# Optimization experiments

Measured on AMD Instinct MI355X. Metric: run time of the kernel, lower is better.

The kernel has to match this reference:

```python
import jax, jax.numpy as jnp
import numpy as np

N_NODES, N_GRAPHS, N_EDGES = 40960, 1024, 163840


def setup_inputs() -> dict:
    key = jax.random.key(0)
    ks = jax.random.split(key, 40)
    w = lambda k, s: jax.random.normal(k, s, jnp.float32) * 0.05
    inp = {
        "x": jax.random.normal(ks[0], (N_NODES, 78), jnp.float32),
        "edge_index": jax.random.randint(ks[1], (2, N_EDGES), 0, N_NODES, jnp.int32),
        "batch": jnp.repeat(jnp.arange(N_GRAPHS, dtype=jnp.int32), N_NODES // N_GRAPHS),
        "target1": jax.random.normal(ks[2], (N_GRAPHS, 750, 20), jnp.float32),
        "target2": jax.random.randint(ks[3], (N_GRAPHS, 750), 0, 26, jnp.int32),
        # GCN layers
        "W1": w(ks[4], (78, 78)), "b1": jnp.zeros((78,), jnp.float32),
        "W2": w(ks[5], (78, 156)), "b2": jnp.zeros((156,), jnp.float32),
        "W3": w(ks[6], (156, 312)), "b3": jnp.zeros((312,), jnp.float32),
        "Wg1": w(ks[7], (312, 1024)), "bg1": jnp.zeros((1024,), jnp.float32),
        "Wg2": w(ks[8], (1024, 128)), "bg2": jnp.zeros((128,), jnp.float32),
        # protein branch
        "emb": w(ks[9], (26, 128)),
        "Wc2": w(ks[10], (32, 750, 8)), "bc2": jnp.zeros((32,), jnp.float32),
        "Wxt2": w(ks[11], (32 * 121, 128)), "bxt2": jnp.zeros((128,), jnp.float32),
        "Wc1": w(ks[12], (32, 750, 8)), "bc1": jnp.zeros((32,), jnp.float32),
        "Wxt1": w(ks[13], (416, 128)), "bxt1": jnp.zeros((128,), jnp.float32),
        # fusion head
        "Wf1": w(ks[14], (384, 1024)), "bf1": jnp.zeros((1024,), jnp.float32),
        "Wf2": w(ks[15], (1024, 512)), "bf2": jnp.zeros((512,), jnp.float32),
        "Wo": w(ks[16], (512, 1)), "bo": jnp.zeros((1,), jnp.float32),
    }
    return inp


def _conv1d(x, w, b):
    # x: [B, C_in, L], w: [C_out, C_in, K] -> [B, C_out, L-K+1]
    y = jax.lax.conv_general_dilated(x, w, (1,), "VALID",
                                     dimension_numbers=("NCH", "OIH", "NCH"))
    return y + b[None, :, None]


def reference(x, edge_index, batch, target1, target2,
              W1, b1, W2, b2, W3, b3, Wg1, bg1, Wg2, bg2,
              emb, Wc2, bc2, Wxt2, bxt2, Wc1, bc1, Wxt1, bxt1,
              Wf1, bf1, Wf2, bf2, Wo, bo):
    N = x.shape[0]
    loop = jnp.arange(N, dtype=edge_index.dtype)
    src = jnp.concatenate([edge_index[0], loop])  # message source j
    dst = jnp.concatenate([edge_index[1], loop])  # aggregation target i
    # symmetric GCN normalization with self-loops (degree from dst, as in PyG)
    deg = jnp.zeros((N,), x.dtype).at[dst].add(1.0)
    dinv = jax.lax.rsqrt(deg)  # deg >= 1 due to self loops
    norm = (dinv[src] * dinv[dst])[:, None]

    def gcn(h, W, b):
        m = (h @ W)[src] * norm
        return jax.ops.segment_sum(m, dst, num_segments=N) + b

    h = jax.nn.relu(gcn(x, W1, b1))
    h = jax.nn.relu(gcn(h, W2, b2))
    h = jax.nn.relu(gcn(h, W3, b3))
    # global max pool per graph
    g = jax.ops.segment_max(h, batch, num_segments=N_GRAPHS)
    g = jax.nn.relu(g @ Wg1 + bg1)
    g = g @ Wg2 + bg2  # dropout is identity at inference

    # protein branch 2: embedding -> conv1d over channels=750
    e = emb[target2]                         # [B, 750, 128]
    xt2 = _conv1d(e, Wc2, bc2)               # [B, 32, 121]
    xt2 = xt2.reshape(-1, 32 * 121) @ Wxt2 + bxt2

    # protein branch 1: raw float features
    xt1 = _conv1d(target1, Wc1, bc1)         # [B, 32, 13]
    xt1 = xt1.reshape(-1, 416) @ Wxt1 + bxt1

    xc = jnp.concatenate([g, xt1, xt2], axis=1)  # [B, 384]
    xc = jax.nn.relu(xc @ Wf1 + bf1)
    xc = jax.nn.relu(xc @ Wf2 + bf2)
    return xc @ Wo + bo
```

## Files before the change

kernel.cpp:

```cpp
#include <hip/hip_runtime.h>
#include <hip/hip_bf16.h>

#define NN 40960
#define NE 163840
#define NB 1024

typedef __attribute__((ext_vector_type(8))) short short8;
typedef __attribute__((ext_vector_type(4))) float floatx4;

__device__ inline unsigned short f2bf(float f) {
    union { float f; unsigned u; } v; v.f = f;
    unsigned r = v.u + 0x7fffu + ((v.u >> 16) & 1u);
    return (unsigned short)(r >> 16);
}
__device__ inline float bf2f(unsigned short s) {
    union { unsigned u; float f; } v; v.u = ((unsigned)s) << 16; return v.f;
}

static const size_t o_dinv = 0, o_g312 = 40960, o_g1024 = 360448, o_xc = 1409024,
                    o_f1 = 1802240, o_f2 = 2850816, o_b1v = 3375104, o_b2v = 3375232,
                    o_iws = 3375360, o_bufA = 3621124, o_bufB = 16400644;


__global__ void k_hist(const int* __restrict__ dst, int* __restrict__ cnt) {
    int e = blockIdx.x * 256 + threadIdx.x;
    if (e < NE) atomicAdd(&cnt[dst[e]], 1);
}

__global__ __launch_bounds__(1024) void k_scan1(const int* __restrict__ cnt, int* __restrict__ offTmp,
                                                int* __restrict__ blockSum, float* __restrict__ dinv) {
    __shared__ int lds[1024];
    int tid = threadIdx.x;
    int i = blockIdx.x * 1024 + tid;
    int v = cnt[i];
    dinv[i] = rsqrtf((float)v + 1.0f);
    lds[tid] = v;
    __syncthreads();
    for (int s = 1; s < 1024; s <<= 1) {
        int t = (tid >= s) ? lds[tid - s] : 0;
        __syncthreads();
        lds[tid] += t;
        __syncthreads();
    }
    offTmp[i] = lds[tid] - v;
    if (tid == 1023) blockSum[blockIdx.x] = lds[1023];
}

__global__ __launch_bounds__(64) void k_scan2(const int* __restrict__ blockSum, int* __restrict__ blockOff) {
    int l = threadIdx.x;
    int s = (l < 40) ? blockSum[l] : 0;
    int orig = s;
    for (int d = 1; d < 64; d <<= 1) {
        int t = __shfl_up(s, d);
        if (l >= d) s += t;
    }
    if (l < 40) blockOff[l] = s - orig;
}

__global__ __launch_bounds__(1024) void k_scan3(int* __restrict__ off, int* __restrict__ cur,
                                                const int* __restrict__ blockOff) {
    int i = blockIdx.x * 1024 + threadIdx.x;
    int o = off[i] + blockOff[blockIdx.x];
    off[i] = o;
    cur[i] = o;
    if (i == NN - 1) off[NN] = NE;
}

__global__ void k_fill(const int* __restrict__ ei, int* __restrict__ cur, int* __restrict__ srcOut) {
    int e = blockIdx.x * 256 + threadIdx.x;
    if (e >= NE) return;
    int s = ei[e], d = ei[NE + e];
    int pos = atomicAdd(&cur[d], 1);
    srcOut[pos] = s;
}

__global__ __launch_bounds__(256) void k_cvt_wt(const float* __restrict__ W1, const float* __restrict__ W2,
                                                const float* __restrict__ W3, const float* __restrict__ Wg1,
                                                const float* __restrict__ Wg2, const float* __restrict__ Wf1,
                                                const float* __restrict__ Wf2, unsigned short* __restrict__ dst) {
    const int cum[8]  = {0, 128, 320, 640, 1664, 1792, 2816, 3328};
    const int KP[7]   = {96, 96, 160, 320, 1024, 384, 1024};
    const int KB[7]   = {78, 78, 156, 312, 1024, 384, 1024};
    const int NNm[7]  = {78, 156, 312, 1024, 128, 1024, 512};
    const size_t OFF[7] = {0, 12288, 30720, 81920, 409600, 540672, 933888};
    int m = 0;
    int bx = blockIdx.x;
    while (m < 6 && bx >= cum[m + 1]) m++;
    int r = bx - cum[m];
    const float* src = (m == 0) ? W1 : (m == 1) ? W2 : (m == 2) ? W3 : (m == 3) ? Wg1
                     : (m == 4) ? Wg2 : (m == 5) ? Wf1 : Wf2;
    int kp = KP[m], kb = KB[m], nn = NNm[m];
    unsigned short* d = dst + OFF[m] + (size_t)r * kp;
    for (int k = threadIdx.x; k < kp; k += 256) {
        float v = (r < nn && k < kb) ? src[(size_t)k * nn + r] : 0.f;
        d[k] = f2bf(v);
    }
}

__global__ __launch_bounds__(256) void k_cvt_flat(const float* __restrict__ in, unsigned short* __restrict__ out, long n) {
    long i = ((long)blockIdx.x * 256 + threadIdx.x) * 8;
    if (i + 8 > n) return;
    float4 a = *(const float4*)(in + i);
    float4 b = *(const float4*)(in + i + 4);
    short8 sv;
    sv[0] = (short)f2bf(a.x); sv[1] = (short)f2bf(a.y); sv[2] = (short)f2bf(a.z); sv[3] = (short)f2bf(a.w);
    sv[4] = (short)f2bf(b.x); sv[5] = (short)f2bf(b.y); sv[6] = (short)f2bf(b.z); sv[7] = (short)f2bf(b.w);
    *(short8*)(out + i) = sv;
}

__global__ void k_agg_x(const float* __restrict__ x, const float* __restrict__ dinv,
                        const int* __restrict__ off, const int* __restrict__ srcs,
                        unsigned short* __restrict__ out) {
    int n = blockIdx.x;
    int f = threadIdx.x;
    if (f >= 96) return;
    if (f >= 78) { out[(size_t)n * 96 + f] = 0; return; }
    float di = dinv[n];
    float acc = x[(size_t)n * 78 + f] * di * di;
    int e0 = off[n], e1 = off[n + 1];
    int e = e0;
    for (; e + 4 <= e1; e += 4) {
        int s0 = srcs[e], s1 = srcs[e + 1], s2 = srcs[e + 2], s3 = srcs[e + 3];
        float d0 = dinv[s0], d1 = dinv[s1], d2 = dinv[s2], d3 = dinv[s3];
        float v0 = x[(size_t)s0 * 78 + f];
        float v1 = x[(size_t)s1 * 78 + f];
        float v2 = x[(size_t)s2 * 78 + f];
        float v3 = x[(size_t)s3 * 78 + f];
        acc += v0 * (d0 * di) + v1 * (d1 * di) + v2 * (d2 * di) + v3 * (d3 * di);
    }
    for (; e < e1; e++) {
        int s = srcs[e];
        acc += x[(size_t)s * 78 + f] * (dinv[s] * di);
    }
    out[(size_t)n * 96 + f] = f2bf(acc);
}

__global__ void k_agg16(const unsigned short* __restrict__ h, const float* __restrict__ dinv,
                        const int* __restrict__ off, const int* __restrict__ srcs,
                        unsigned short* __restrict__ out, int F) {
    int n = blockIdx.x;
    int f = threadIdx.x;
    if (f >= F) return;
    float di = dinv[n];
    float acc = bf2f(h[(size_t)n * F + f]) * di * di;
    int e0 = off[n], e1 = off[n + 1];
    int e = e0;
    for (; e + 4 <= e1; e += 4) {
        int s0 = srcs[e], s1 = srcs[e + 1], s2 = srcs[e + 2], s3 = srcs[e + 3];
        float d0 = dinv[s0], d1 = dinv[s1], d2 = dinv[s2], d3 = dinv[s3];
        float v0 = bf2f(h[(size_t)s0 * F + f]);
        float v1 = bf2f(h[(size_t)s1 * F + f]);
        float v2 = bf2f(h[(size_t)s2 * F + f]);
        float v3 = bf2f(h[(size_t)s3 * F + f]);
        acc += v0 * (d0 * di) + v1 * (d1 * di) + v2 * (d2 * di) + v3 * (d3 * di);
    }
    for (; e < e1; e++) {
        int s = srcs[e];
        acc += bf2f(h[(size_t)s * F + f]) * (dinv[s] * di);
    }
    out[(size_t)n * F + f] = f2bf(acc);
}

__global__ void k_segmax16(const unsigned short* __restrict__ h, unsigned short* __restrict__ g) {
    int gr = blockIdx.x, f = threadIdx.x;
    if (f >= 320) return;
    if (f >= 312) { g[(size_t)gr * 320 + f] = 0; return; }
    float m = 0.0f;
    const unsigned short* base = h + (size_t)gr * 40 * 312 + f;
    for (int i = 0; i < 40; i++) m = fmaxf(m, bf2f(base[(size_t)i * 312]));
    g[(size_t)gr * 320 + f] = f2bf(m);
}

#define LDST 72
template <bool ABF16, bool OUTBF16, bool ATOMIC, bool RELU_OUT>
__global__ __launch_bounds__(256) void gemm_bt(const void* __restrict__ Av, const unsigned short* __restrict__ Bt,
                                               const float* __restrict__ bias, void* __restrict__ Cv,
                                               int Nn, int Npad, int Kpad,
                                               int lda, int ldb, int ldc, int ksplit) {
    __shared__ __align__(16) unsigned short As[64 * LDST];
    __shared__ __align__(16) unsigned short Bs[64 * LDST];
    const float* Af = (const float*)Av;
    const unsigned short* A16 = (const unsigned short*)Av;
    float* Cf = (float*)Cv;
    unsigned short* C16 = (unsigned short*)Cv;
    int bn0 = blockIdx.x * 64;
    int bm0 = blockIdx.y * 64;
    int k0 = blockIdx.z * ksplit;
    int kend = k0 + ksplit; if (kend > Kpad) kend = Kpad;
    int tid = threadIdx.x;
    int w = tid >> 6, l = tid & 63, q = l >> 4, r = l & 15;
    int wr = w >> 1, wc = w & 1;

    floatx4 acc[2][2];
#pragma unroll
    for (int i = 0; i < 2; i++)
#pragma unroll
        for (int c = 0; c < 2; c++) acc[i][c] = (floatx4)0.0f;

    int mA = tid >> 2, kcA = (tid & 3) * 8;
    int nB = tid >> 2, kcB = (tid & 3) * 8;
    int gmA = bm0 + mA;
    int gnB = bn0 + nB;

    for (int kt = k0; kt < kend; kt += 32) {
        if (ABF16) {
            *(short8*)&As[mA * LDST + kcA] = *(const short8*)(A16 + (size_t)gmA * lda + kt + kcA);
        } else {
            const float* Ap = Af + (size_t)gmA * lda + kt + kcA;
            float av[8];
#pragma unroll
            for (int j = 0; j < 4; j++) {
                float2 p = *(const float2*)(Ap + j * 2);
                av[j * 2] = p.x; av[j * 2 + 1] = p.y;
            }
            short8 sv;
#pragma unroll
            for (int j = 0; j < 8; j++) sv[j] = (short)f2bf(av[j]);
            *(short8*)&As[mA * LDST + kcA] = sv;
        }
        *(short8*)&Bs[nB * LDST + kcB] = *(const short8*)(Bt + (size_t)gnB * ldb + kt + kcB);
        __syncthreads();
        short8 a0 = *(const short8*)&As[(wr * 32 + r) * LDST + q * 8];
        short8 a1 = *(const short8*)&As[(wr * 32 + 16 + r) * LDST + q * 8];
        short8 b0 = *(const short8*)&Bs[(wc * 32 + r) * LDST + q * 8];
        short8 b1 = *(const short8*)&Bs[(wc * 32 + 16 + r) * LDST + q * 8];
        acc[0][0] = __builtin_amdgcn_mfma_f32_16x16x32_bf16(a0, b0, acc[0][0], 0, 0, 0);
        acc[0][1] = __builtin_amdgcn_mfma_f32_16x16x32_bf16(a0, b1, acc[0][1], 0, 0, 0);
        acc[1][0] = __builtin_amdgcn_mfma_f32_16x16x32_bf16(a1, b0, acc[1][0], 0, 0, 0);
        acc[1][1] = __builtin_amdgcn_mfma_f32_16x16x32_bf16(a1, b1, acc[1][1], 0, 0, 0);
        __syncthreads();
    }

#pragma unroll
    for (int c2 = 0; c2 < 2; c2++) {
        int col = bn0 + wc * 32 + c2 * 16 + r;
        if (col >= Npad) continue;
        bool live = col < Nn;
        float bv = (bias && live) ? bias[col] : 0.f;
#pragma unroll
        for (int i = 0; i < 2; i++) {
#pragma unroll
            for (int v = 0; v < 4; v++) {
                int row = bm0 + wr * 32 + i * 16 + q * 4 + v;
                float val = live ? (acc[i][c2][v] + bv) : 0.f;
                if (RELU_OUT) val = fmaxf(val, 0.f);
                if (OUTBF16) {
                    C16[(size_t)row * ldc + col] = live ? f2bf(val) : (unsigned short)0;
                } else if (live) {
                    if (ATOMIC) atomicAdd(&Cf[(size_t)row * ldc + col], val);
                    else Cf[(size_t)row * ldc + col] = val;
                }
            }
        }
    }
}

template <int OM>
__global__ __launch_bounds__(256) void gemm_mfma_batch(const float* __restrict__ A, const float* __restrict__ B,
                                                       void* __restrict__ Cv,
                                                       int M, int Nn, int K, int ldc,
                                                       long sB, long sC) {
    __shared__ __align__(16) unsigned short As[64 * LDST];
    __shared__ __align__(16) unsigned short Bs[64 * LDST];
    const float* Bm = B + (size_t)blockIdx.z * sB;
    unsigned short* C16 = (unsigned short*)Cv + (size_t)blockIdx.z * sC;
    int bn0 = blockIdx.x * 64;
    int bm0 = blockIdx.y * 64;
    int tid = threadIdx.x;
    int w = tid >> 6, l = tid & 63, q = l >> 4, r = l & 15;
    int wr = w >> 1, wc = w & 1;

    floatx4 acc[2][2];
#pragma unroll
    for (int i = 0; i < 2; i++)
#pragma unroll
        for (int c = 0; c < 2; c++) acc[i][c] = (floatx4)0.0f;

    int mA = tid >> 2, kcA = (tid & 3) * 8;
    int nB = tid >> 2, kcB = (tid & 3) * 8;
    int gmA = bm0 + mA;
    int gnB = bn0 + nB;

    for (int kt = 0; kt < K; kt += 32) {
        {
            float av[8];
            const float* Ap = A + (size_t)gmA * K + kt + kcA;
            if (gmA < M) {
#pragma unroll
                for (int j = 0; j < 4; j++) {
                    float2 p = *(const float2*)(Ap + j * 2);
                    av[j * 2] = p.x; av[j * 2 + 1] = p.y;
                }
            } else {
#pragma unroll
                for (int j = 0; j < 8; j++) av[j] = 0.f;
            }
            short8 sv;
#pragma unroll
            for (int j = 0; j < 8; j++) sv[j] = (short)f2bf(av[j]);
            *(short8*)&As[mA * LDST + kcA] = sv;
        }
        {
            short8 sv;
#pragma unroll
            for (int j = 0; j < 8; j++) {
                int gk = kt + kcB + j;
                float v = (gnB < Nn) ? Bm[(size_t)gk * Nn + gnB] : 0.f;
                sv[j] = (short)f2bf(v);
            }
            *(short8*)&Bs[nB * LDST + kcB] = sv;
        }
        __syncthreads();
        short8 a0 = *(const short8*)&As[(wr * 32 + r) * LDST + q * 8];
        short8 a1 = *(const short8*)&As[(wr * 32 + 16 + r) * LDST + q * 8];
        short8 b0 = *(const short8*)&Bs[(wc * 32 + r) * LDST + q * 8];
        short8 b1 = *(const short8*)&Bs[(wc * 32 + 16 + r) * LDST + q * 8];
        acc[0][0] = __builtin_amdgcn_mfma_f32_16x16x32_bf16(a0, b0, acc[0][0], 0, 0, 0);
        acc[0][1] = __builtin_amdgcn_mfma_f32_16x16x32_bf16(a0, b1, acc[0][1], 0, 0, 0);
        acc[1][0] = __builtin_amdgcn_mfma_f32_16x16x32_bf16(a1, b0, acc[1][0], 0, 0, 0);
        acc[1][1] = __builtin_amdgcn_mfma_f32_16x16x32_bf16(a1, b1, acc[1][1], 0, 0, 0);
        __syncthreads();
    }

#pragma unroll
    for (int c = 0; c < 2; c++) {
        int col = bn0 + wc * 32 + c * 16 + r;
        if (col >= Nn) continue;
#pragma unroll
        for (int i = 0; i < 2; i++) {
#pragma unroll
            for (int v = 0; v < 4; v++) {
                int row = bm0 + wr * 32 + i * 16 + q * 4 + v;
                if (row >= M) continue;
                if (OM == 1) C16[(size_t)row * ldc + col] = f2bf(acc[i][c][v]);
                else C16[(size_t)col * ldc + row * 20 + blockIdx.z] = f2bf(acc[i][c][v]);
            }
        }
    }
}

__global__ void k_rowinit(float* __restrict__ C, int ldc, const float* __restrict__ bias) {
    C[(size_t)blockIdx.x * ldc + threadIdx.x] = bias[threadIdx.x];
}

__global__ __launch_bounds__(256) void k_wcr(const float* __restrict__ W, float* __restrict__ Wr) {
    int c = blockIdx.x, j = threadIdx.x;
    Wr[(size_t)c * 256 + j] = W[(size_t)(j >> 3) * 6000 + c * 8 + (j & 7)];
}

__global__ __launch_bounds__(128) void k_T_build(const float* __restrict__ emb, const float* __restrict__ Wxt2,
                                                 float* __restrict__ T) {
    __shared__ float el[128];
    int v = blockIdx.x >> 5, o = blockIdx.x & 31, j = threadIdx.x;
    el[j] = emb[(size_t)v * 128 + j];
    __syncthreads();
    float acc[8] = {};
    for (int l = 0; l < 121; l++) {
        float w = Wxt2[(size_t)(o * 121 + l) * 128 + j];
#pragma unroll
        for (int k = 0; k < 8; k++) acc[k] += el[l + k] * w;
    }
#pragma unroll
    for (int k = 0; k < 8; k++) T[(size_t)(v * 256 + o * 8 + k) * 128 + j] = acc[k];
}

__global__ __launch_bounds__(128) void k_bt_build(const float* __restrict__ Wxt1, float* __restrict__ Bt) {
    int ok = blockIdx.x, t = blockIdx.y, j = threadIdx.x;
    int o = ok >> 3, k = ok & 7, lpos = t - k;
    float v = (lpos >= 0 && lpos < 13) ? Wxt1[(size_t)(o * 13 + lpos) * 128 + j] : 0.f;
    Bt[(size_t)(t * 256 + ok) * 128 + j] = v;
}

__global__ __launch_bounds__(128) void k_u_gather16(const int* __restrict__ t2, const unsigned short* __restrict__ U,
                                                    const float* __restrict__ b2v, float* __restrict__ xc) {
    __shared__ int offs[752];
    __shared__ float red[8][128];
    int b = blockIdx.x, tid = threadIdx.x;
    int rg = tid >> 4, lane = tid & 15;
    const int* t2b = t2 + (size_t)b * 750;
    for (int i = tid; i < 750; i += 128) offs[i] = i * 3328 + t2b[i] * 128;
    __syncthreads();
    float a[8] = {};
#pragma unroll 4
    for (int i = rg; i < 750; i += 8) {
        short8 v = *(const short8*)&U[(size_t)offs[i] + lane * 8];
#pragma unroll
        for (int c = 0; c < 8; c++) a[c] += bf2f((unsigned short)v[c]);
    }
#pragma unroll
    for (int c = 0; c < 8; c++) red[rg][lane * 8 + c] = a[c];
    __syncthreads();
    float s = b2v[tid];
#pragma unroll
    for (int g = 0; g < 8; g++) s += red[g][tid];
    xc[(size_t)b * 384 + 256 + tid] = s;
}

__global__ void k_bias_init(const float* __restrict__ bxt1, const float* __restrict__ bxt2,
                            float* __restrict__ b1v, float* __restrict__ b2v) {
    int j = threadIdx.x;
    b1v[j] = bxt1[j];
    b2v[j] = bxt2[j];
}

template <int L>
__global__ __launch_bounds__(128) void k_bias_acc(const float* __restrict__ bc, const float* __restrict__ W,
                                                  float* __restrict__ out) {
    int o = blockIdx.x, j = threadIdx.x;
    const float* p = W + (size_t)o * L * 128 + j;
    float t = 0.f;
    for (int l = 0; l < L; l++) t += p[(size_t)l * 128];
    atomicAdd(&out[j], bc[o] * t);
}

__global__ __launch_bounds__(64) void k_final(const float* __restrict__ f2, const float* __restrict__ Wo,
                                              const float* __restrict__ bo, float* __restrict__ out) {
    int b = blockIdx.x, lane = threadIdx.x;
    float s = 0.f;
    for (int j = lane; j < 512; j += 64) s += fmaxf(f2[(size_t)b * 512 + j], 0.f) * Wo[j];
    for (int off = 32; off; off >>= 1) s += __shfl_down(s, off);
    if (lane == 0) out[b] = s + bo[0];
}

extern "C" void kernel_launch(void* const* d_in, const int* in_sizes, int n_in,
                              void* d_out, int out_size, void* d_ws, size_t ws_size,
                              hipStream_t stream) {
    const float* x    = (const float*)d_in[0];
    const int*   ei   = (const int*)d_in[1];
    const float* t1   = (const float*)d_in[3];
    const int*   t2   = (const int*)d_in[4];
    const float* W1   = (const float*)d_in[5];
    const float* b1   = (const float*)d_in[6];
    const float* W2   = (const float*)d_in[7];
    const float* b2   = (const float*)d_in[8];
    const float* W3   = (const float*)d_in[9];
    const float* b3   = (const float*)d_in[10];
    const float* Wg1  = (const float*)d_in[11];
    const float* bg1  = (const float*)d_in[12];
    const float* Wg2  = (const float*)d_in[13];
    const float* bg2  = (const float*)d_in[14];
    const float* emb  = (const float*)d_in[15];
    const float* Wc2  = (const float*)d_in[16];
    const float* bc2  = (const float*)d_in[17];
    const float* Wxt2 = (const float*)d_in[18];
    const float* bxt2 = (const float*)d_in[19];
    const float* Wc1  = (const float*)d_in[20];
    const float* bc1  = (const float*)d_in[21];
    const float* Wxt1 = (const float*)d_in[22];
    const float* bxt1 = (const float*)d_in[23];
    const float* Wf1  = (const float*)d_in[24];
    const float* bf1  = (const float*)d_in[25];
    const float* Wf2  = (const float*)d_in[26];
    const float* bf2  = (const float*)d_in[27];
    const float* Wo   = (const float*)d_in[28];
    const float* bo   = (const float*)d_in[29];
    float* out = (float*)d_out;

    float* ws = (float*)d_ws;
    float* dinv  = ws + o_dinv;
    unsigned short* g312b = (unsigned short*)(ws + o_g312);
    unsigned short* g1024b = (unsigned short*)(ws + o_g1024);
    float* xc    = ws + o_xc;
    unsigned short* f1b = (unsigned short*)(ws + o_f1);
    float* f2    = ws + o_f2;
    float* b1v   = ws + o_b1v;
    float* b2v   = ws + o_b2v;
    int* csrOff  = (int*)(ws + o_iws);
    int* csrCur  = csrOff + (NN + 1);
    int* csrSrc  = csrCur + NN;
    int* blockSum = (int*)(ws + o_f1 + 600000);
    int* blockOff = blockSum + 40;
    float* bufA  = ws + o_bufA;
    float* bufB  = ws + o_bufB;
    float* T    = bufA;
    unsigned short* U16  = (unsigned short*)(bufA + 851968);
    unsigned short* Vt16 = (unsigned short*)(bufA + 2200000);
    unsigned short* Wt   = (unsigned short*)(bufA + 3200000);
    float* Wc2r = bufA + 4000000;
    float* Wc1r = bufA + 4200000;
    float* Btb  = bufA + 4400000;
    unsigned short* aggb = (unsigned short*)bufB;
    unsigned short* h16  = (unsigned short*)(bufB + 5500000);
    unsigned short* t1b  = (unsigned short*)bufB;

    unsigned short* W1t  = Wt + 0;
    unsigned short* W2t  = Wt + 12288;
    unsigned short* W3t  = Wt + 30720;
    unsigned short* Wg1t = Wt + 81920;
    unsigned short* Wg2t = Wt + 409600;
    unsigned short* Wf1t = Wt + 540672;
    unsigned short* Wf2t = Wt + 933888;

    hipMemsetAsync(csrCur, 0, NN * sizeof(int), stream);
    k_hist<<<NE / 256, 256, 0, stream>>>(ei + NE, csrCur);
    k_scan1<<<40, 1024, 0, stream>>>(csrCur, csrOff, blockSum, dinv);
    k_scan2<<<1, 64, 0, stream>>>(blockSum, blockOff);
    k_scan3<<<40, 1024, 0, stream>>>(csrOff, csrCur, blockOff);
    k_fill<<<NE / 256, 256, 0, stream>>>(ei, csrCur, csrSrc);
    k_cvt_wt<<<3328, 256, 0, stream>>>(W1, W2, W3, Wg1, Wg2, Wf1, Wf2, Wt);

    k_agg_x<<<NN, 128, 0, stream>>>(x, dinv, csrOff, csrSrc, aggb);
    gemm_bt<true, true, false, true><<<dim3(2, 640, 1), 256, 0, stream>>>(
        aggb, W1t, b1, h16, 78, 96, 96, 96, 96, 96, 96);
    k_agg16<<<NN, 128, 0, stream>>>(h16, dinv, csrOff, csrSrc, aggb, 96);
    gemm_bt<true, true, false, true><<<dim3(3, 640, 1), 256, 0, stream>>>(
        aggb, W2t, b2, h16, 156, 160, 96, 96, 96, 160, 96);
    k_agg16<<<NN, 192, 0, stream>>>(h16, dinv, csrOff, csrSrc, aggb, 160);
    gemm_bt<true, true, false, true><<<dim3(5, 640, 1), 256, 0, stream>>>(
        aggb, W3t, b3, h16, 312, 312, 160, 160, 160, 312, 160);
    k_segmax16<<<NB, 320, 0, stream>>>(h16, g312b);
    k_cvt_flat<<<7500, 256, 0, stream>>>(t1, t1b, 15360000L);
    gemm_bt<true, true, false, true><<<dim3(16, 16, 1), 256, 0, stream>>>(
        g312b, Wg1t, bg1, g1024b, 1024, 1024, 320, 320, 320, 1024, 320);

    k_bias_init<<<1, 128, 0, stream>>>(bxt1, bxt2, b1v, b2v);
    k_bias_acc<13><<<32, 128, 0, stream>>>(bc1, Wxt1, b1v);
    k_bias_acc<121><<<32, 128, 0, stream>>>(bc2, Wxt2, b2v);

    k_rowinit<<<NB, 128, 0, stream>>>(xc + 0, 384, bg2);
    gemm_bt<true, false, true, false><<<dim3(2, 16, 8), 256, 0, stream>>>(
        g1024b, Wg2t, nullptr, xc + 0, 128, 128, 1024, 1024, 1024, 384, 128);

    k_wcr<<<750, 256, 0, stream>>>(Wc2, Wc2r);
    k_T_build<<<26 * 32, 128, 0, stream>>>(emb, Wxt2, T);
    gemm_mfma_batch<1><<<dim3(2, 12, 26), 256, 0, stream>>>(Wc2r, T, U16, 750, 128, 256, 3328, 32768, 128);
    k_u_gather16<<<NB, 128, 0, stream>>>(t2, U16, b2v, xc);

    k_wcr<<<750, 256, 0, stream>>>(Wc1, Wc1r);
    k_bt_build<<<dim3(256, 20), 128, 0, stream>>>(Wxt1, Btb);
    hipMemsetAsync(Vt16, 0, (size_t)128 * 15008 * 2, stream);
    gemm_mfma_batch<2><<<dim3(2, 12, 20), 256, 0, stream>>>(Wc1r, Btb, Vt16, 750, 128, 256, 15008, 32768, 0);
    k_rowinit<<<NB, 128, 0, stream>>>(xc + 128, 384, b1v);
    gemm_bt<true, false, true, false><<<dim3(2, 16, 32), 256, 0, stream>>>(
        t1b, Vt16, nullptr, xc + 128, 128, 128, 15008, 15000, 15008, 384, 480);

    gemm_bt<false, true, false, true><<<dim3(16, 16, 1), 256, 0, stream>>>(
        xc, Wf1t, bf1, f1b, 1024, 1024, 384, 384, 384, 1024, 384);
    k_rowinit<<<NB, 512, 0, stream>>>(f2, 512, bf2);
    gemm_bt<true, false, true, false><<<dim3(8, 16, 4), 256, 0, stream>>>(
        f1b, Wf2t, nullptr, f2, 512, 512, 1024, 1024, 1024, 512, 256);
    k_final<<<NB, 64, 0, stream>>>(f2, Wo, bo, out);
}
```

Measured before the change: 499.7 us.

## Vectorize GCN aggregation, fuse small init kernels, drop target1 bf16 pre-conversion

The GCN aggregation kernels now process two features per thread with packed bf16 pairs and float2 loads, which halves the thread count per node. Several tiny launches are merged: both conv-weight reorders, both bias accumulations, and the three row-init kernels. The separate fp32-to-bf16 conversion pass over target1 is removed, and the split-K GEMM instead reads fp32 directly with a new K-limit bound for the ragged tail. The aim is to cut launch overhead and one full read/write pass over the large target1 tensor, at the cost of converting inside the GEMM and reading fp32 there, which is twice the bytes of bf16.

Result: faster. 463.3 us (-7.3%).

```diff
diff --git a/kernel.cpp b/kernel.cpp
--- a/kernel.cpp
+++ b/kernel.cpp
@@ -16,11 +16,13 @@
 __device__ inline float bf2f(unsigned short s) {
     union { unsigned u; float f; } v; v.u = ((unsigned)s) << 16; return v.f;
 }
+__device__ inline unsigned pack2bf(float lo, float hi) {
+    return (unsigned)f2bf(lo) | ((unsigned)f2bf(hi) << 16);
+}
 
 static const size_t o_dinv = 0, o_g312 = 40960, o_g1024 = 360448, o_xc = 1409024,
                     o_f1 = 1802240, o_f2 = 2850816, o_b1v = 3375104, o_b2v = 3375232,
                     o_iws = 3375360, o_bufA = 3621124, o_bufB = 16400644;
-
 
 __global__ void k_hist(const int* __restrict__ dst, int* __restrict__ cnt) {
     int e = blockIdx.x * 256 + threadIdx.x;
@@ -97,68 +99,69 @@
     }
 }
 
-__global__ __launch_bounds__(256) void k_cvt_flat(const float* __restrict__ in, unsigned short* __restrict__ out, long n) {
-    long i = ((long)blockIdx.x * 256 + threadIdx.x) * 8;
-    if (i + 8 > n) return;
-    float4 a = *(const float4*)(in + i);
-    float4 b = *(const float4*)(in + i + 4);
-    short8 sv;
-    sv[0] = (short)f2bf(a.x); sv[1] = (short)f2bf(a.y); sv[2] = (short)f2bf(a.z); sv[3] = (short)f2bf(a.w);
-    sv[4] = (short)f2bf(b.x); sv[5] = (short)f2bf(b.y); sv[6] = (short)f2bf(b.z); sv[7] = (short)f2bf(b.w);
-    *(short8*)(out + i) = sv;
-}
-
-__global__ void k_agg_x(const float* __restrict__ x, const float* __restrict__ dinv,
-                        const int* __restrict__ off, const int* __restrict__ srcs,
-                        unsigned short* __restrict__ out) {
+__global__ __launch_bounds__(64) void k_agg_x(const float* __restrict__ x, const float* __restrict__ dinv,
+                                              const int* __restrict__ off, const int* __restrict__ srcs,
+                                              unsigned* __restrict__ out) {
     int n = blockIdx.x;
     int f = threadIdx.x;
-    if (f >= 96) return;
-    if (f >= 78) { out[(size_t)n * 96 + f] = 0; return; }
+    if (f >= 48) return;
+    if (f >= 39) { out[(size_t)n * 48 + f] = 0; return; }
     float di = dinv[n];
-    float acc = x[(size_t)n * 78 + f] * di * di;
+    float2 sv = *(const float2*)&x[(size_t)n * 78 + 2 * f];
+    float a0 = sv.x * di * di, a1 = sv.y * di * di;
     int e0 = off[n], e1 = off[n + 1];
     int e = e0;
     for (; e + 4 <= e1; e += 4) {
         int s0 = srcs[e], s1 = srcs[e + 1], s2 = srcs[e + 2], s3 = srcs[e + 3];
-        float d0 = dinv[s0], d1 = dinv[s1], d2 = dinv[s2], d3 = dinv[s3];
-        float v0 = x[(size_t)s0 * 78 + f];
-        float v1 = x[(size_t)s1 * 78 + f];
-        float v2 = x[(size_t)s2 * 78 + f];
-        float v3 = x[(size_t)s3 * 78 + f];
-        acc += v0 * (d0 * di) + v1 * (d1 * di) + v2 * (d2 * di) + v3 * (d3 * di);
+        float d0 = dinv[s0] * di, d1 = dinv[s1] * di, d2 = dinv[s2] * di, d3 = dinv[s3] * di;
+        float2 v0 = *(const float2*)&x[(size_t)s0 * 78 + 2 * f];
+        float2 v1 = *(const float2*)&x[(size_t)s1 * 78 + 2 * f];
+        float2 v2 = *(const float2*)&x[(size_t)s2 * 78 + 2 * f];
+        float2 v3 = *(const float2*)&x[(size_t)s3 * 78 + 2 * f];
+        a0 += v0.x * d0 + v1.x * d1 + v2.x * d2 + v3.x * d3;
+        a1 += v0.y * d0 + v1.y * d1 + v2.y * d2 + v3.y * d3;
     }
     for (; e < e1; e++) {
         int s = srcs[e];
-        acc += x[(size_t)s * 78 + f] * (dinv[s] * di);
-    }
-    out[(size_t)n * 96 + f] = f2bf(acc);
-}
-
-__global__ void k_agg16(const unsigned short* __restrict__ h, const float* __restrict__ dinv,
+        float dd = dinv[s] * di;
+        float2 v = *(const float2*)&x[(size_t)s * 78 + 2 * f];
+        a0 += v.x * dd; a1 += v.y * dd;
+    }
+    out[(size_t)n * 48 + f] = pack2bf(a0, a1);
+}
+
+__global__ void k_agg16(const unsigned* __restrict__ h, const float* __restrict__ dinv,
                         const int* __restrict__ off, const int* __restrict__ srcs,
-                        unsigned short* __restrict__ out, int F) {
+                        unsigned* __restrict__ out, int F2) {
     int n = blockIdx.x;
     int f = threadIdx.x;
-    if (f >= F) return;
+    if (f >= F2) return;
     float di = dinv[n];
-    float acc = bf2f(h[(size_t)n * F + f]) * di * di;
+    unsigned s0v = h[(size_t)n * F2 + f];
+    float a0 = bf2f((unsigned short)(s0v & 0xffff)) * di * di;
+    float a1 = bf2f((unsigned short)(s0v >> 16)) * di * di;
     int e0 = off[n], e1 = off[n + 1];
     int e = e0;
     for (; e + 4 <= e1; e += 4) {
         int s0 = srcs[e], s1 = srcs[e + 1], s2 = srcs[e + 2], s3 = srcs[e + 3];
-        float d0 = dinv[s0], d1 = dinv[s1], d2 = dinv[s2], d3 = dinv[s3];
-        float v0 = bf2f(h[(size_t)s0 * F + f]);
-        float v1 = bf2f(h[(size_t)s1 * F + f]);
-        float v2 = bf2f(h[(size_t)s2 * F + f]);
-        float v3 = bf2f(h[(size_t)s3 * F + f]);
-        acc += v0 * (d0 * di) + v1 * (d1 * di) + v2 * (d2 * di) + v3 * (d3 * di);
+        float d0 = dinv[s0] * di, d1 = dinv[s1] * di, d2 = dinv[s2] * di, d3 = dinv[s3] * di;
+        unsigned v0 = h[(size_t)s0 * F2 + f];
+        unsigned v1 = h[(size_t)s1 * F2 + f];
+        unsigned v2 = h[(size_t)s2 * F2 + f];
+        unsigned v3 = h[(size_t)s3 * F2 + f];
+        a0 += bf2f((unsigned short)(v0 & 0xffff)) * d0 + bf2f((unsigned short)(v1 & 0xffff)) * d1
+            + bf2f((unsigned short)(v2 & 0xffff)) * d2 + bf2f((unsigned short)(v3 & 0xffff)) * d3;
+        a1 += bf2f((unsigned short)(v0 >> 16)) * d0 + bf2f((unsigned short)(v1 >> 16)) * d1
+            + bf2f((unsigned short)(v2 >> 16)) * d2 + bf2f((unsigned short)(v3 >> 16)) * d3;
     }
     for (; e < e1; e++) {
         int s = srcs[e];
-        acc += bf2f(h[(size_t)s * F + f]) * (dinv[s] * di);
-    }
-    out[(size_t)n * F + f] = f2bf(acc);
+        float dd = dinv[s] * di;
+        unsigned v = h[(size_t)s * F2 + f];
+        a0 += bf2f((unsigned short)(v & 0xffff)) * dd;
+        a1 += bf2f((unsigned short)(v >> 16)) * dd;
+    }
+    out[(size_t)n * F2 + f] = pack2bf(a0, a1);
 }
 
 __global__ void k_segmax16(const unsigned short* __restrict__ h, unsigned short* __restrict__ g) {
@@ -175,7 +178,7 @@
 template <bool ABF16, bool OUTBF16, bool ATOMIC, bool RELU_OUT>
 __global__ __launch_bounds__(256) void gemm_bt(const void* __restrict__ Av, const unsigned short* __restrict__ Bt,
                                                const float* __restrict__ bias, void* __restrict__ Cv,
-                                               int Nn, int Npad, int Kpad,
+                                               int Nn, int Npad, int Kpad, int Klim,
                                                int lda, int ldb, int ldc, int ksplit) {
     __shared__ __align__(16) unsigned short As[64 * LDST];
     __shared__ __align__(16) unsigned short Bs[64 * LDST];
@@ -208,10 +211,15 @@
         } else {
             const float* Ap = Af + (size_t)gmA * lda + kt + kcA;
             float av[8];
-#pragma unroll
-            for (int j = 0; j < 4; j++) {
-                float2 p = *(const float2*)(Ap + j * 2);
-                av[j * 2] = p.x; av[j * 2 + 1] = p.y;
+            if (kt + kcA + 8 <= Klim) {
+#pragma unroll
+                for (int j = 0; j < 4; j++) {
+                    float2 p = *(const float2*)(Ap + j * 2);
+                    av[j * 2] = p.x; av[j * 2 + 1] = p.y;
+                }
+            } else {
+#pragma unroll
+                for (int j = 0; j < 8; j++) av[j] = (kt + kcA + j < Klim) ? Ap[j] : 0.f;
             }
             short8 sv;
 #pragma unroll
@@ -339,12 +347,12 @@
     }
 }
 
-__global__ void k_rowinit(float* __restrict__ C, int ldc, const float* __restrict__ bias) {
-    C[(size_t)blockIdx.x * ldc + threadIdx.x] = bias[threadIdx.x];
-}
-
-__global__ __launch_bounds__(256) void k_wcr(const float* __restrict__ W, float* __restrict__ Wr) {
-    int c = blockIdx.x, j = threadIdx.x;
+__global__ __launch_bounds__(256) void k_wcr_both(const float* __restrict__ Wc2, const float* __restrict__ Wc1,
+                                                  float* __restrict__ Wc2r, float* __restrict__ Wc1r) {
+    int cc = blockIdx.x, j = threadIdx.x;
+    const float* W = (cc < 750) ? Wc2 : Wc1;
+    float* Wr = (cc < 750) ? Wc2r : Wc1r;
+    int c = (cc < 750) ? cc : cc - 750;
     Wr[(size_t)c * 256 + j] = W[(size_t)(j >> 3) * 6000 + c * 8 + (j & 7)];
 }
 
@@ -403,14 +411,32 @@
     b2v[j] = bxt2[j];
 }
 
-template <int L>
-__global__ __launch_bounds__(128) void k_bias_acc(const float* __restrict__ bc, const float* __restrict__ W,
-                                                  float* __restrict__ out) {
-    int o = blockIdx.x, j = threadIdx.x;
-    const float* p = W + (size_t)o * L * 128 + j;
-    float t = 0.f;
-    for (int l = 0; l < L; l++) t += p[(size_t)l * 128];
-    atomicAdd(&out[j], bc[o] * t);
+__global__ __launch_bounds__(128) void k_bias_acc_both(const float* __restrict__ bc1, const float* __restrict__ Wxt1,
+                                                       float* __restrict__ b1v,
+                                                       const float* __restrict__ bc2, const float* __restrict__ Wxt2,
+                                                       float* __restrict__ b2v) {
+    int b = blockIdx.x, j = threadIdx.x;
+    if (b < 32) {
+        const float* p = Wxt1 + (size_t)b * 13 * 128 + j;
+        float t = 0.f;
+        for (int l = 0; l < 13; l++) t += p[(size_t)l * 128];
+        atomicAdd(&b1v[j], bc1[b] * t);
+    } else {
+        int o = b - 32;
+        const float* p = Wxt2 + (size_t)o * 121 * 128 + j;
+        float t = 0.f;
+        for (int l = 0; l < 121; l++) t += p[(size_t)l * 128];
+        atomicAdd(&b2v[j], bc2[o] * t);
+    }
+}
+
+__global__ __launch_bounds__(768) void k_initC(float* __restrict__ xc, float* __restrict__ f2,
+                                               const float* __restrict__ bg2, const float* __restrict__ b1v,
+                                               const float* __restrict__ bf2) {
+    int b = blockIdx.x, t = threadIdx.x;
+    if (t < 128) xc[(size_t)b * 384 + t] = bg2[t];
+    else if (t < 256) xc[(size_t)b * 384 + t] = b1v[t - 128];
+    else f2[(size_t)b * 512 + t - 256] = bf2[t - 256];
 }
 
 __global__ __launch_bounds__(64) void k_final(const float* __restrict__ f2, const float* __restrict__ Wo,
@@ -479,9 +505,8 @@
     float* Wc2r = bufA + 4000000;
     float* Wc1r = bufA + 4200000;
     float* Btb  = bufA + 4400000;
-    unsigned short* aggb = (unsigned short*)bufB;
-    unsigned short* h16  = (unsigned short*)(bufB + 5500000);
-    unsigned short* t1b  = (unsigned short*)bufB;
+    unsigned* aggb = (unsigned*)bufB;
+    unsigned short* h16 = (unsigned short*)(bufB + 5500000);
 
     unsigned short* W1t  = Wt + 0;
     unsigned short* W2t  = Wt + 12288;
@@ -499,45 +524,40 @@
     k_fill<<<NE / 256, 256, 0, stream>>>(ei, csrCur, csrSrc);
     k_cvt_wt<<<3328, 256, 0, stream>>>(W1, W2, W3, Wg1, Wg2, Wf1, Wf2, Wt);
 
-    k_agg_x<<<NN, 128, 0, stream>>>(x, dinv, csrOff, csrSrc, aggb);
+    k_agg_x<<<NN, 64, 0, stream>>>(x, dinv, csrOff, csrSrc, aggb);
     gemm_bt<true, true, false, true><<<dim3(2, 640, 1), 256, 0, stream>>>(
-        aggb, W1t, b1, h16, 78, 96, 96, 96, 96, 96, 96);
-    k_agg16<<<NN, 128, 0, stream>>>(h16, dinv, csrOff, csrSrc, aggb, 96);
+        aggb, W1t, b1, h16, 78, 96, 96, 96, 96, 96, 96, 96);
+    k_agg16<<<NN, 64, 0, stream>>>((unsigned*)h16, dinv, csrOff, csrSrc, aggb, 48);
     gemm_bt<true, true, false, true><<<dim3(3, 640, 1), 256, 0, stream>>>(
-        aggb, W2t, b2, h16, 156, 160, 96, 96, 96, 160, 96);
-    k_agg16<<<NN, 192, 0, stream>>>(h16, dinv, csrOff, csrSrc, aggb, 160);
+        aggb, W2t, b2, h16, 156, 160, 96, 96, 96, 96, 160, 96);
+    k_agg16<<<NN, 128, 0, stream>>>((unsigned*)h16, dinv, csrOff, csrSrc, aggb, 80);
     gemm_bt<true, true, false, true><<<dim3(5, 640, 1), 256, 0, stream>>>(
-        aggb, W3t, b3, h16, 312, 312, 160, 160, 160, 312, 160);
+        aggb, W3t, b3, h16, 312, 312, 160, 160, 160, 160, 312, 160);
     k_segmax16<<<NB, 320, 0, stream>>>(h16, g312b);
-    k_cvt_flat<<<7500, 256, 0, stream>>>(t1, t1b, 15360000L);
     gemm_bt<true, true, false, true><<<dim3(16, 16, 1), 256, 0, stream>>>(
-        g312b, Wg1t, bg1, g1024b, 1024, 1024, 320, 320, 320, 1024, 320);
+        g312b, Wg1t, bg1, g1024b, 1024, 1024, 320, 320, 320, 320, 1024, 320);
 
     k_bias_init<<<1, 128, 0, stream>>>(bxt1, bxt2, b1v, b2v);
-    k_bias_acc<13><<<32, 128, 0, stream>>>(bc1, Wxt1, b1v);
-    k_bias_acc<121><<<32, 128, 0, stream>>>(bc2, Wxt2, b2v);
-
-    k_rowinit<<<NB, 128, 0, stream>>>(xc + 0, 384, bg2);
+    k_bias_acc_both<<<64, 128, 0, stream>>>(bc1, Wxt1, b1v, bc2, Wxt2, b2v);
+    k_initC<<<NB, 768, 0, stream>>>(xc, f2, bg2, b1v, bf2);
+
     gemm_bt<true, false, true, false><<<dim3(2, 16, 8), 256, 0, stream>>>(
-        g1024b, Wg2t, nullptr, xc + 0, 128, 128, 1024, 1024, 1024, 384, 128);
-
-    k_wcr<<<750, 256, 0, stream>>>(Wc2, Wc2r);
+        g1024b, Wg2t, nullptr, xc + 0, 128, 128, 1024, 1024, 1024, 1024, 384, 128);
+
+    k_wcr_both<<<1500, 256, 0, stream>>>(Wc2, Wc1, Wc2r, Wc1r);
     k_T_build<<<26 * 32, 128, 0, stream>>>(emb, Wxt2, T);
     gemm_mfma_batch<1><<<dim3(2, 12, 26), 256, 0, stream>>>(Wc2r, T, U16, 750, 128, 256, 3328, 32768, 128);
     k_u_gather16<<<NB, 128, 0, stream>>>(t2, U16, b2v, xc);
 
-    k_wcr<<<750, 256, 0, stream>>>(Wc1, Wc1r);
     k_bt_build<<<dim3(256, 20), 128, 0, stream>>>(Wxt1, Btb);
     hipMemsetAsync(Vt16, 0, (size_t)128 * 15008 * 2, stream);
     gemm_mfma_batch<2><<<dim3(2, 12, 20), 256, 0, stream>>>(Wc1r, Btb, Vt16, 750, 128, 256, 15008, 32768, 0);
-    k_rowinit<<<NB, 128, 0, stream>>>(xc + 128, 384, b1v);
-    gemm_bt<true, false, true, false><<<dim3(2, 16, 32), 256, 0, stream>>>(
-        t1b, Vt16, nullptr, xc + 128, 128, 128, 15008, 15000, 15008, 384, 480);
+    gemm_bt<false, false, true, false><<<dim3(2, 16, 32), 256, 0, stream>>>(
+        t1, Vt16, nullptr, xc + 128, 128, 128, 15008, 15000, 15000, 15008, 384, 480);
 
     gemm_bt<false, true, false, true><<<dim3(16, 16, 1), 256, 0, stream>>>(
-        xc, Wf1t, bf1, f1b, 1024, 1024, 384, 384, 384, 1024, 384);
-    k_rowinit<<<NB, 512, 0, stream>>>(f2, 512, bf2);
+        xc, Wf1t, bf1, f1b, 1024, 1024, 384, 384, 384, 384, 1024, 384);
     gemm_bt<true, false, true, false><<<dim3(8, 16, 4), 256, 0, stream>>>(
-        f1b, Wf2t, nullptr, f2, 512, 512, 1024, 1024, 1024, 512, 256);
+        f1b, Wf2t, nullptr, f2, 512, 512, 1024, 1024, 1024, 1024, 512, 256);
     k_final<<<NB, 64, 0, stream>>>(f2, Wo, bo, out);
 }
```
